# Performance work log

Hardware: AMD Instinct MI355X
Metric: run time of the kernel (lower is better)

Reference implementation:

```python
import jax, jax.numpy as jnp
import numpy as np

B, T, D = 4, 2048, 512
H, DK = 8, 64  # n_head, d_kv; inner_dim = H*DK = 512


def setup_inputs() -> dict:
    key = jax.random.key(0)
    ks = jax.random.split(key, 6)
    s = 1.0 / np.sqrt(D)
    return {
        "x": jax.random.normal(ks[0], (B, T, D), dtype=jnp.float32),
        "mask": jnp.zeros((B, 1, 1, T), dtype=jnp.float32),
        "position_bias": jax.random.normal(ks[1], (1, H, T, T), dtype=jnp.float32),
        "Wq": jax.random.normal(ks[2], (D, D), dtype=jnp.float32) * s,
        "Wk": jax.random.normal(ks[3], (D, D), dtype=jnp.float32) * s,
        "Wv": jax.random.normal(ks[4], (D, D), dtype=jnp.float32) * s,
        "Wo": jax.random.normal(ks[5], (D, D), dtype=jnp.float32) * s,
    }


def reference(x, mask, position_bias, Wq, Wk, Wv, Wo):
    # Linear projections (torch nn.Linear: y = x @ W.T), split into heads.
    q = (x @ Wq.T).reshape(B, T, H, DK).transpose(0, 2, 1, 3)  # [B,H,T,DK]
    k = (x @ Wk.T).reshape(B, T, H, DK).transpose(0, 2, 1, 3)  # [B,H,S,DK]
    v = (x @ Wv.T).reshape(B, T, H, DK).transpose(0, 2, 1, 3)  # [B,H,S,DK]
    # T5: no 1/sqrt(d_k) scaling; additive position bias + mask before softmax.
    scores = jnp.einsum("bhtd,bhsd->bhts", q, k) + position_bias + mask
    attn = jax.nn.softmax(scores.astype(jnp.float32), axis=-1).astype(q.dtype)
    # dropout is identity at inference
    y = jnp.einsum("bhts,bhsd->bhtd", attn, v)  # [B,H,T,DK]
    y = y.transpose(0, 2, 1, 3).reshape(B, T, H * DK)
    return y @ Wo.T
```

## Files before the change

kernel.cpp:

```cpp
#include <hip/hip_runtime.h>
#include <stdint.h>

typedef unsigned short u16;
typedef __attribute__((ext_vector_type(8))) _Float16 half8;
typedef __attribute__((ext_vector_type(4))) float f32x4;

#define L2E 1.4426950408889634f

#define NTOK 8192
#define DIM  512
#define TT   2048

__device__ __forceinline__ u16 f2h(float f) {
  _Float16 h = (_Float16)f;
  return __builtin_bit_cast(u16, h);
}

__device__ __forceinline__ void async16(const void* g, void* l) {
  __builtin_amdgcn_global_load_lds(
      (const __attribute__((address_space(1))) unsigned int*)g,
      (__attribute__((address_space(3))) unsigned int*)l, 16, 0, 0);
}

__global__ __launch_bounds__(256) void k_convert(
    const float* __restrict__ x, const float* __restrict__ wq,
    const float* __restrict__ wk, const float* __restrict__ wv,
    const float* __restrict__ wo, u16* __restrict__ xb) {
  size_t i = ((size_t)blockIdx.x * 256 + threadIdx.x) * 8;
  const float* src;
  u16* dst;
  size_t off;
  if (i < 4194304) {
    src = x; dst = xb; off = i;
  } else {
    size_t j = i - 4194304;
    int w = (int)(j >> 18);
    off = j & 262143;
    src = (w == 0) ? wq : (w == 1) ? wk : (w == 2) ? wv : wo;
    dst = xb + 4194304 + (size_t)w * 262144;
  }
  float4 a = *(const float4*)(src + off);
  float4 b = *(const float4*)(src + off + 4);
  uint4 pk;
  pk.x = (unsigned)f2h(a.x) | ((unsigned)f2h(a.y) << 16);
  pk.y = (unsigned)f2h(a.z) | ((unsigned)f2h(a.w) << 16);
  pk.z = (unsigned)f2h(b.x) | ((unsigned)f2h(b.y) << 16);
  pk.w = (unsigned)f2h(b.z) | ((unsigned)f2h(b.w) << 16);
  *(uint4*)(dst + off) = pk;
}

template <bool VSWAP>
__global__ __launch_bounds__(256) void k_proj(
    const u16* __restrict__ A, const u16* __restrict__ Wb,
    u16* __restrict__ Db) {
  const int tid = threadIdx.x;
  const int wave = tid >> 6, lane = tid & 63;
  const int quad = lane >> 4, l16 = lane & 15;
  const int wr = wave >> 1, wc = wave & 1;
  const int m0 = blockIdx.x * 128, n0 = blockIdx.y * 128;

  const u16* W;
  u16* D;
  if (VSWAP) {
    W = Wb + 2 * 262144;
    D = Db + 2 * (size_t)4194304;
  } else {
    int z = blockIdx.z;
    W = Wb + (size_t)z * 262144;
    D = Db + (size_t)z * 4194304;
  }

  __shared__ __align__(16) u16 As[128 * 64];
  __shared__ __align__(16) u16 Bs[128 * 64];

  f32x4 acc[4][4];
  for (int rt = 0; rt < 4; ++rt)
    for (int ct = 0; ct < 4; ++ct) acc[rt][ct] = (f32x4){0.f, 0.f, 0.f, 0.f};

  for (int kb = 0; kb < 8; ++kb) {
    const int k0 = kb * 64;
    for (int r = 0; r < 4; ++r) {
      int cid = r * 256 + tid;
      int row = cid >> 3, cl = cid & 7, cg = cl ^ (row & 7);
      async16(A + (size_t)(m0 + row) * DIM + k0 + cg * 8,
              &As[(r * 256 + wave * 64) * 8]);
    }
    for (int r = 0; r < 4; ++r) {
      int cid = r * 256 + tid;
      int row = cid >> 3, cl = cid & 7, cg = cl ^ (row & 7);
      async16(W + (size_t)(n0 + row) * DIM + k0 + cg * 8,
              &Bs[(r * 256 + wave * 64) * 8]);
    }
    __syncthreads();
    for (int kc = 0; kc < 2; ++kc) {
      half8 af[4], wf[4];
      for (int rt = 0; rt < 4; ++rt) {
        int row = wr * 64 + rt * 16 + l16;
        int c = (kc * 4 + quad) ^ (row & 7);
        af[rt] = *(const half8*)&As[row * 64 + c * 8];
      }
      for (int ct = 0; ct < 4; ++ct) {
        int row = wc * 64 + ct * 16 + l16;
        int c = (kc * 4 + quad) ^ (row & 7);
        wf[ct] = *(const half8*)&Bs[row * 64 + c * 8];
      }
      for (int rt = 0; rt < 4; ++rt)
        for (int ct = 0; ct < 4; ++ct)
          acc[rt][ct] = VSWAP
              ? __builtin_amdgcn_mfma_f32_16x16x32_f16(wf[ct], af[rt],
                                                       acc[rt][ct], 0, 0, 0)
              : __builtin_amdgcn_mfma_f32_16x16x32_f16(af[rt], wf[ct],
                                                       acc[rt][ct], 0, 0, 0);
    }
    __syncthreads();
  }

  for (int rt = 0; rt < 4; ++rt)
    for (int ct = 0; ct < 4; ++ct)
      for (int reg = 0; reg < 4; ++reg) {
        float v = acc[rt][ct][reg];
        if (!VSWAP) {
          int gm = m0 + wr * 64 + rt * 16 + quad * 4 + reg;
          int gn = n0 + wc * 64 + ct * 16 + l16;
          int bb = gm >> 11, t = gm & 2047, hh = gn >> 6, dk = gn & 63;
          D[(((size_t)(bb * 8 + hh) * TT + t) << 6) + dk] = f2h(v);
        } else {
          int feat = n0 + wc * 64 + ct * 16 + quad * 4 + reg;
          int tok  = m0 + wr * 64 + rt * 16 + l16;
          int bb = tok >> 11, t = tok & 2047, hh = feat >> 6, dk = feat & 63;
          D[(((size_t)(bb * 8 + hh) << 6) + dk) * TT + t] = f2h(v);
        }
      }
}

__global__ __launch_bounds__(256) void k_ogemm(
    const u16* __restrict__ A, const u16* __restrict__ W,
    float* __restrict__ Df) {
  const int tid = threadIdx.x;
  const int wave = tid >> 6, lane = tid & 63;
  const int quad = lane >> 4, l16 = lane & 15;
  const int wr = wave >> 1, wc = wave & 1;
  const int m0 = blockIdx.x * 64, n0 = blockIdx.y * 128;

  __shared__ __align__(16) u16 As[64 * 64];
  __shared__ __align__(16) u16 Bs[128 * 64];

  f32x4 acc[2][4];
  for (int rt = 0; rt < 2; ++rt)
    for (int ct = 0; ct < 4; ++ct) acc[rt][ct] = (f32x4){0.f, 0.f, 0.f, 0.f};

  for (int kb = 0; kb < 8; ++kb) {
    const int k0 = kb * 64;
    for (int r = 0; r < 2; ++r) {
      int cid = r * 256 + tid;
      int row = cid >> 3, cl = cid & 7, cg = cl ^ (row & 7);
      async16(A + (size_t)(m0 + row) * DIM + k0 + cg * 8,
              &As[(r * 256 + wave * 64) * 8]);
    }
    for (int r = 0; r < 4; ++r) {
      int cid = r * 256 + tid;
      int row = cid >> 3, cl = cid & 7, cg = cl ^ (row & 7);
      async16(W + (size_t)(n0 + row) * DIM + k0 + cg * 8,
              &Bs[(r * 256 + wave * 64) * 8]);
    }
    __syncthreads();
    for (int kc = 0; kc < 2; ++kc) {
      half8 af[2], wf[4];
      for (int rt = 0; rt < 2; ++rt) {
        int row = wr * 32 + rt * 16 + l16;
        int c = (kc * 4 + quad) ^ (row & 7);
        af[rt] = *(const half8*)&As[row * 64 + c * 8];
      }
      for (int ct = 0; ct < 4; ++ct) {
        int row = wc * 64 + ct * 16 + l16;
        int c = (kc * 4 + quad) ^ (row & 7);
        wf[ct] = *(const half8*)&Bs[row * 64 + c * 8];
      }
      for (int rt = 0; rt < 2; ++rt)
        for (int ct = 0; ct < 4; ++ct)
          acc[rt][ct] = __builtin_amdgcn_mfma_f32_16x16x32_f16(
              af[rt], wf[ct], acc[rt][ct], 0, 0, 0);
    }
    __syncthreads();
  }

  for (int rt = 0; rt < 2; ++rt)
    for (int ct = 0; ct < 4; ++ct)
      for (int reg = 0; reg < 4; ++reg) {
        int gm = m0 + wr * 32 + rt * 16 + quad * 4 + reg;
        int gn = n0 + wc * 64 + ct * 16 + l16;
        Df[(size_t)gm * DIM + gn] = acc[rt][ct][reg];
      }
}

__global__ __launch_bounds__(256, 4) void k_attn(
    const u16* __restrict__ Q, const u16* __restrict__ K,
    const u16* __restrict__ Vt, const float* __restrict__ bias,
    const float* __restrict__ mask, u16* __restrict__ Y) {
  const int tid = threadIdx.x;
  const int wv = tid >> 6;
  const int lane = tid & 63;
  const int quad = lane >> 4;
  const int l16 = lane & 15;

  const int bx = blockIdx.x;
  const int bh = bx >> 5;
  const int qt = bx & 31;
  const int b = bh >> 3, h = bh & 7;
  const int q0 = qt * 64;

  __shared__ __align__(16) u16 Ks[64 * 64];
  __shared__ __align__(16) u16 Vs[64 * 64];
  __shared__ __align__(16) u16 Pl[64 * 72];

  const int qrow = q0 + wv * 16 + l16;
  half8 qf[2];
  {
    size_t qoff = ((size_t)bh * TT + qrow) * 64;
    qf[0] = *(const half8*)(Q + qoff + quad * 8);
    qf[1] = *(const half8*)(Q + qoff + 32 + quad * 8);
  }

  const float* brow = bias + (size_t)h * TT * TT + (size_t)qrow * TT + quad * 4;
  const float* mrow = mask + (size_t)b * TT + quad * 4;

  float m_i = -1e30f, l_i = 0.f;
  f32x4 oacc[4];
  for (int ct = 0; ct < 4; ++ct) oacc[ct] = (f32x4){0.f, 0.f, 0.f, 0.f};

  f32x4 bL[4];
  for (int ct = 0; ct < 4; ++ct) bL[ct] = *(const f32x4*)(brow + ct * 16);

  for (int st = 0; st < 32; ++st) {
    const int s0 = st * 64;
    for (int r = 0; r < 2; ++r) {
      int cid = r * 256 + tid;
      int row = cid >> 3, cl = cid & 7, cg = cl ^ (row & 7);
      async16(K + ((size_t)bh * TT + s0 + row) * 64 + cg * 8,
              &Ks[(r * 256 + wv * 64) * 8]);
      async16(Vt + ((size_t)(bh * 64 + row)) * TT + s0 + cg * 8,
              &Vs[(r * 256 + wv * 64) * 8]);
    }
    f32x4 mL[4];
    for (int ct = 0; ct < 4; ++ct)
      mL[ct] = *(const f32x4*)(mrow + s0 + ct * 16);
    __syncthreads();

    f32x4 sacc[4];
    for (int ct = 0; ct < 4; ++ct) sacc[ct] = (f32x4){0.f, 0.f, 0.f, 0.f};
    __builtin_amdgcn_s_setprio(1);
    for (int kc = 0; kc < 2; ++kc) {
      half8 kf[4];
      for (int ct = 0; ct < 4; ++ct) {
        int row = ct * 16 + l16;
        int c = (kc * 4 + quad) ^ (row & 7);
        kf[ct] = *(const half8*)&Ks[row * 64 + c * 8];
      }
      for (int ct = 0; ct < 4; ++ct)
        sacc[ct] = __builtin_amdgcn_mfma_f32_16x16x32_f16(kf[ct], qf[kc],
                                                          sacc[ct], 0, 0, 0);
    }
    __builtin_amdgcn_s_setprio(0);

    float sv[4][4];
    for (int ct = 0; ct < 4; ++ct)
      for (int reg = 0; reg < 4; ++reg)
        sv[ct][reg] = sacc[ct][reg] + bL[ct][reg] + mL[ct][reg];

    {
      int sn = (st < 31) ? s0 + 64 : 0;
      for (int ct = 0; ct < 4; ++ct)
        bL[ct] = *(const f32x4*)(brow + sn + ct * 16);
    }

    float mc[4];
    for (int ct = 0; ct < 4; ++ct)
      mc[ct] = fmaxf(fmaxf(sv[ct][0], sv[ct][1]), fmaxf(sv[ct][2], sv[ct][3]));
    float mx = fmaxf(fmaxf(mc[0], mc[1]), fmaxf(mc[2], mc[3]));
    mx = fmaxf(mx, __shfl_xor(mx, 16));
    mx = fmaxf(mx, __shfl_xor(mx, 32));
    float mnew = fmaxf(m_i, mx);
    float alpha = __builtin_amdgcn_exp2f((m_i - mnew) * L2E);
    float nl2e = mnew * L2E;
    float rs = 0.f;
    for (int ct = 0; ct < 4; ++ct)
      for (int reg = 0; reg < 4; ++reg) {
        float p = __builtin_amdgcn_exp2f(sv[ct][reg] * L2E - nl2e);
        sv[ct][reg] = p;
        rs += p;
      }
    rs += __shfl_xor(rs, 16);
    rs += __shfl_xor(rs, 32);
    l_i = l_i * alpha + rs;
    m_i = mnew;
    for (int ct = 0; ct < 4; ++ct) {
      oacc[ct][0] *= alpha; oacc[ct][1] *= alpha;
      oacc[ct][2] *= alpha; oacc[ct][3] *= alpha;
    }

    for (int ct = 0; ct < 4; ++ct) {
      uint2 pk;
      pk.x = (unsigned)f2h(sv[ct][0]) | ((unsigned)f2h(sv[ct][1]) << 16);
      pk.y = (unsigned)f2h(sv[ct][2]) | ((unsigned)f2h(sv[ct][3]) << 16);
      *(uint2*)&Pl[(wv * 16 + l16) * 72 + ct * 16 + quad * 4] = pk;
    }
    asm volatile("s_waitcnt lgkmcnt(0)" ::: "memory");
    __builtin_amdgcn_sched_barrier(0);

    __builtin_amdgcn_s_setprio(1);
    for (int kc = 0; kc < 2; ++kc) {
      half8 pf = *(const half8*)&Pl[(wv * 16 + l16) * 72 + kc * 32 + quad * 8];
      half8 vf[4];
      for (int ct = 0; ct < 4; ++ct) {
        int row = ct * 16 + l16;
        int c = (kc * 4 + quad) ^ (row & 7);
        vf[ct] = *(const half8*)&Vs[row * 64 + c * 8];
      }
      for (int ct = 0; ct < 4; ++ct)
        oacc[ct] = __builtin_amdgcn_mfma_f32_16x16x32_f16(vf[ct], pf,
                                                          oacc[ct], 0, 0, 0);
    }
    __builtin_amdgcn_s_setprio(0);
    __syncthreads();
  }

  float inv = 1.f / l_i;
  size_t ybase = ((size_t)(b * TT + qrow)) * DIM + h * 64 + quad * 4;
  for (int ct = 0; ct < 4; ++ct) {
    uint2 pk;
    pk.x = (unsigned)f2h(oacc[ct][0] * inv) |
           ((unsigned)f2h(oacc[ct][1] * inv) << 16);
    pk.y = (unsigned)f2h(oacc[ct][2] * inv) |
           ((unsigned)f2h(oacc[ct][3] * inv) << 16);
    *(uint2*)(Y + ybase + ct * 16) = pk;
  }
}

extern "C" void kernel_launch(void* const* d_in, const int* in_sizes, int n_in,
                              void* d_out, int out_size, void* d_ws, size_t ws_size,
                              hipStream_t stream) {
  const float* x    = (const float*)d_in[0];
  const float* mask = (const float*)d_in[1];
  const float* bias = (const float*)d_in[2];
  const float* Wq   = (const float*)d_in[3];
  const float* Wk   = (const float*)d_in[4];
  const float* Wv   = (const float*)d_in[5];
  const float* Wo   = (const float*)d_in[6];
  (void)Wk; (void)Wv;

  u16* xb  = (u16*)d_ws;
  u16* wb  = xb + 4194304;
  u16* qkv = wb + 4 * 262144;
  u16* yb  = qkv + 3 * (size_t)4194304;

  k_convert<<<2560, 256, 0, stream>>>(x, Wq, Wk, Wv, Wo, xb);
  k_proj<false><<<dim3(64, 4, 2), 256, 0, stream>>>(xb, wb, qkv);
  k_proj<true><<<dim3(64, 4), 256, 0, stream>>>(xb, wb, qkv);
  k_attn<<<1024, 256, 0, stream>>>(qkv, qkv + 4194304,
                                   qkv + 2 * (size_t)4194304, bias, mask, yb);
  k_ogemm<<<dim3(128, 4), 256, 0, stream>>>(yb, wb + 3 * 262144, (float*)d_out);
}
```

Before: 322.1 us.

## Double-buffer K/V tiles, lazy softmax rescale, swizzle P, reorder blocks by head

The attention kernel now double-buffers the K and V shared-memory tiles, issuing async loads for the next tile before computing on the current one. This removes the load-then-barrier stall at the top of each iteration. Several other changes ride along: the online-softmax rescale of the output and running sum is skipped unless the row max grows by more than 8, and the P scratch buffer uses an XOR swizzle in place of padding. Block indices are also remapped so that consecutive blocks cover different heads of the same batch. The cost is double the K/V shared memory, which may lower occupancy. The lazy rescale lets exponentials exceed 1 (up to about e^8), which stays within fp16 range.

Result: slower. 342.4 us (+6.3%).

```diff
diff --git a/kernel.cpp b/kernel.cpp
--- a/kernel.cpp
+++ b/kernel.cpp
@@ -204,14 +204,16 @@
   const int l16 = lane & 15;
 
   const int bx = blockIdx.x;
-  const int bh = bx >> 5;
-  const int qt = bx & 31;
-  const int b = bh >> 3, h = bh & 7;
+  const int h = bx & 7;
+  const int lid = bx >> 3;
+  const int b = lid >> 5;
+  const int qt = lid & 31;
+  const int bh = b * 8 + h;
   const int q0 = qt * 64;
 
-  __shared__ __align__(16) u16 Ks[64 * 64];
-  __shared__ __align__(16) u16 Vs[64 * 64];
-  __shared__ __align__(16) u16 Pl[64 * 72];
+  __shared__ __align__(16) u16 Ks[2][64 * 64];
+  __shared__ __align__(16) u16 Vs[2][64 * 64];
+  __shared__ __align__(16) u16 Pl[64 * 64];
 
   const int qrow = q0 + wv * 16 + l16;
   half8 qf[2];
@@ -228,101 +230,118 @@
   f32x4 oacc[4];
   for (int ct = 0; ct < 4; ++ct) oacc[ct] = (f32x4){0.f, 0.f, 0.f, 0.f};
 
-  f32x4 bL[4];
-  for (int ct = 0; ct < 4; ++ct) bL[ct] = *(const f32x4*)(brow + ct * 16);
-
-  for (int st = 0; st < 32; ++st) {
-    const int s0 = st * 64;
-    for (int r = 0; r < 2; ++r) {
-      int cid = r * 256 + tid;
-      int row = cid >> 3, cl = cid & 7, cg = cl ^ (row & 7);
-      async16(K + ((size_t)bh * TT + s0 + row) * 64 + cg * 8,
-              &Ks[(r * 256 + wv * 64) * 8]);
-      async16(Vt + ((size_t)(bh * 64 + row)) * TT + s0 + cg * 8,
-              &Vs[(r * 256 + wv * 64) * 8]);
-    }
-    f32x4 mL[4];
-    for (int ct = 0; ct < 4; ++ct)
-      mL[ct] = *(const f32x4*)(mrow + s0 + ct * 16);
-    __syncthreads();
-
-    f32x4 sacc[4];
-    for (int ct = 0; ct < 4; ++ct) sacc[ct] = (f32x4){0.f, 0.f, 0.f, 0.f};
-    __builtin_amdgcn_s_setprio(1);
-    for (int kc = 0; kc < 2; ++kc) {
-      half8 kf[4];
-      for (int ct = 0; ct < 4; ++ct) {
-        int row = ct * 16 + l16;
-        int c = (kc * 4 + quad) ^ (row & 7);
-        kf[ct] = *(const half8*)&Ks[row * 64 + c * 8];
-      }
-      for (int ct = 0; ct < 4; ++ct)
-        sacc[ct] = __builtin_amdgcn_mfma_f32_16x16x32_f16(kf[ct], qf[kc],
-                                                          sacc[ct], 0, 0, 0);
-    }
-    __builtin_amdgcn_s_setprio(0);
-
-    float sv[4][4];
-    for (int ct = 0; ct < 4; ++ct)
-      for (int reg = 0; reg < 4; ++reg)
-        sv[ct][reg] = sacc[ct][reg] + bL[ct][reg] + mL[ct][reg];
-
-    {
-      int sn = (st < 31) ? s0 + 64 : 0;
-      for (int ct = 0; ct < 4; ++ct)
-        bL[ct] = *(const f32x4*)(brow + sn + ct * 16);
-    }
-
-    float mc[4];
-    for (int ct = 0; ct < 4; ++ct)
-      mc[ct] = fmaxf(fmaxf(sv[ct][0], sv[ct][1]), fmaxf(sv[ct][2], sv[ct][3]));
-    float mx = fmaxf(fmaxf(mc[0], mc[1]), fmaxf(mc[2], mc[3]));
-    mx = fmaxf(mx, __shfl_xor(mx, 16));
-    mx = fmaxf(mx, __shfl_xor(mx, 32));
-    float mnew = fmaxf(m_i, mx);
-    float alpha = __builtin_amdgcn_exp2f((m_i - mnew) * L2E);
-    float nl2e = mnew * L2E;
-    float rs = 0.f;
-    for (int ct = 0; ct < 4; ++ct)
-      for (int reg = 0; reg < 4; ++reg) {
-        float p = __builtin_amdgcn_exp2f(sv[ct][reg] * L2E - nl2e);
-        sv[ct][reg] = p;
-        rs += p;
-      }
-    rs += __shfl_xor(rs, 16);
-    rs += __shfl_xor(rs, 32);
-    l_i = l_i * alpha + rs;
-    m_i = mnew;
-    for (int ct = 0; ct < 4; ++ct) {
-      oacc[ct][0] *= alpha; oacc[ct][1] *= alpha;
-      oacc[ct][2] *= alpha; oacc[ct][3] *= alpha;
-    }
-
-    for (int ct = 0; ct < 4; ++ct) {
-      uint2 pk;
-      pk.x = (unsigned)f2h(sv[ct][0]) | ((unsigned)f2h(sv[ct][1]) << 16);
-      pk.y = (unsigned)f2h(sv[ct][2]) | ((unsigned)f2h(sv[ct][3]) << 16);
-      *(uint2*)&Pl[(wv * 16 + l16) * 72 + ct * 16 + quad * 4] = pk;
-    }
-    asm volatile("s_waitcnt lgkmcnt(0)" ::: "memory");
-    __builtin_amdgcn_sched_barrier(0);
-
-    __builtin_amdgcn_s_setprio(1);
-    for (int kc = 0; kc < 2; ++kc) {
-      half8 pf = *(const half8*)&Pl[(wv * 16 + l16) * 72 + kc * 32 + quad * 8];
-      half8 vf[4];
-      for (int ct = 0; ct < 4; ++ct) {
-        int row = ct * 16 + l16;
-        int c = (kc * 4 + quad) ^ (row & 7);
-        vf[ct] = *(const half8*)&Vs[row * 64 + c * 8];
-      }
-      for (int ct = 0; ct < 4; ++ct)
-        oacc[ct] = __builtin_amdgcn_mfma_f32_16x16x32_f16(vf[ct], pf,
-                                                          oacc[ct], 0, 0, 0);
-    }
-    __builtin_amdgcn_s_setprio(0);
-    __syncthreads();
-  }
+  const int prow = wv * 16 + l16;
+  const int r7x = (l16 & 7) << 4;
+  char* plb = (char*)Pl + prow * 128;
+
+#define STAGE(BUF, S0)                                                  \
+  for (int r = 0; r < 2; ++r) {                                         \
+    int cid = r * 256 + tid;                                            \
+    int row = cid >> 3, cl = cid & 7, cg = cl ^ (row & 7);              \
+    async16(K + ((size_t)bh * TT + (S0) + row) * 64 + cg * 8,           \
+            &Ks[BUF][(r * 256 + wv * 64) * 8]);                         \
+    async16(Vt + ((size_t)(bh * 64 + row)) * TT + (S0) + cg * 8,        \
+            &Vs[BUF][(r * 256 + wv * 64) * 8]);                         \
+  }
+
+  f32x4 bA[4], bB[4];
+  STAGE(0, 0);
+  for (int ct = 0; ct < 4; ++ct) bA[ct] = *(const f32x4*)(brow + ct * 16);
+  __syncthreads();
+
+#define TILE(ST, CUR, BU, BF)                                               \
+  {                                                                         \
+    const int s0 = (ST) * 64;                                               \
+    if ((ST) < 31) {                                                        \
+      STAGE((CUR) ^ 1, s0 + 64);                                            \
+      for (int ct = 0; ct < 4; ++ct)                                        \
+        BF[ct] = *(const f32x4*)(brow + s0 + 64 + ct * 16);                 \
+    }                                                                       \
+    f32x4 mL[4];                                                            \
+    for (int ct = 0; ct < 4; ++ct)                                          \
+      mL[ct] = *(const f32x4*)(mrow + s0 + ct * 16);                        \
+                                \
+    f32x4 sacc[4];                                                          \
+    for (int ct = 0; ct < 4; ++ct) sacc[ct] = (f32x4){0.f, 0.f, 0.f, 0.f};  \
+    __builtin_amdgcn_s_setprio(1);                                          \
+    for (int kc = 0; kc < 2; ++kc) {                                        \
+      half8 kf[4];                                                          \
+      for (int ct = 0; ct < 4; ++ct) {                                      \
+        int row = ct * 16 + l16;                                            \
+        int c = (kc * 4 + quad) ^ (row & 7);                                \
+        kf[ct] = *(const half8*)&Ks[CUR][row * 64 + c * 8];                 \
+      }                                                                     \
+      for (int ct = 0; ct < 4; ++ct)                                        \
+        sacc[ct] = __builtin_amdgcn_mfma_f32_16x16x32_f16(kf[ct], qf[kc],   \
+                                                          sacc[ct], 0, 0, 0); \
+    }                                                                       \
+    __builtin_amdgcn_s_setprio(0);                                          \
+    float sv[4][4];                                                         \
+    for (int ct = 0; ct < 4; ++ct)                                          \
+      for (int rg = 0; rg < 4; ++rg)                                        \
+        sv[ct][rg] = sacc[ct][rg] + BU[ct][rg] + mL[ct][rg];                \
+                     \
+    float mc0 = fmaxf(fmaxf(sv[0][0], sv[0][1]), fmaxf(sv[0][2], sv[0][3])); \
+    float mc1 = fmaxf(fmaxf(sv[1][0], sv[1][1]), fmaxf(sv[1][2], sv[1][3])); \
+    float mc2 = fmaxf(fmaxf(sv[2][0], sv[2][1]), fmaxf(sv[2][2], sv[2][3])); \
+    float mc3 = fmaxf(fmaxf(sv[3][0], sv[3][1]), fmaxf(sv[3][2], sv[3][3])); \
+    float mx = fmaxf(fmaxf(mc0, mc1), fmaxf(mc2, mc3));                     \
+    mx = fmaxf(mx, __shfl_xor(mx, 16));                                     \
+    mx = fmaxf(mx, __shfl_xor(mx, 32));                                     \
+    if (!__all(mx <= m_i + 8.f)) {                                          \
+      float mnew = fmaxf(m_i, mx);                                          \
+      float alpha = __builtin_amdgcn_exp2f((m_i - mnew) * L2E);             \
+      l_i *= alpha;                                                         \
+      m_i = mnew;                                                           \
+      for (int ct = 0; ct < 4; ++ct) {                                      \
+        oacc[ct][0] *= alpha; oacc[ct][1] *= alpha;                         \
+        oacc[ct][2] *= alpha; oacc[ct][3] *= alpha;                         \
+      }                                                                     \
+    }                                                                       \
+    float nl2e = m_i * L2E;                                                 \
+    float rs = 0.f;                                                         \
+    for (int ct = 0; ct < 4; ++ct)                                          \
+      for (int rg = 0; rg < 4; ++rg) {                                      \
+        float p = __builtin_amdgcn_exp2f(sv[ct][rg] * L2E - nl2e);          \
+        sv[ct][rg] = p;                                                     \
+        rs += p;                                                            \
+      }                                                                     \
+    rs += __shfl_xor(rs, 16);                                               \
+    rs += __shfl_xor(rs, 32);                                               \
+    l_i += rs;                                                              \
+                            \
+    for (int ct = 0; ct < 4; ++ct) {                                        \
+      uint2 pk;                                                             \
+      pk.x = (unsigned)f2h(sv[ct][0]) | ((unsigned)f2h(sv[ct][1]) << 16);   \
+      pk.y = (unsigned)f2h(sv[ct][2]) | ((unsigned)f2h(sv[ct][3]) << 16);   \
+      *(uint2*)(plb + ((ct * 32 + quad * 8) ^ r7x)) = pk;                   \
+    }                                                                       \
+    asm volatile("s_waitcnt lgkmcnt(0)" ::: "memory");                      \
+    __builtin_amdgcn_sched_barrier(0);                                      \
+                            \
+    __builtin_amdgcn_s_setprio(1);                                          \
+    for (int kc = 0; kc < 2; ++kc) {                                        \
+      half8 pf = *(const half8*)(plb + ((kc * 64 + quad * 16) ^ r7x));      \
+      half8 vf[4];                                                          \
+      for (int ct = 0; ct < 4; ++ct) {                                      \
+        int row = ct * 16 + l16;                                            \
+        int c = (kc * 4 + quad) ^ (row & 7);                                \
+        vf[ct] = *(const half8*)&Vs[CUR][row * 64 + c * 8];                 \
+      }                                                                     \
+      for (int ct = 0; ct < 4; ++ct)                                        \
+        oacc[ct] = __builtin_amdgcn_mfma_f32_16x16x32_f16(vf[ct], pf,       \
+                                                          oacc[ct], 0, 0, 0); \
+    }                                                                       \
+    __builtin_amdgcn_s_setprio(0);                                          \
+    __syncthreads();                                                        \
+  }
+
+  for (int st2 = 0; st2 < 16; ++st2) {
+    TILE(2 * st2, 0, bA, bB);
+    TILE(2 * st2 + 1, 1, bB, bA);
+  }
+#undef TILE
+#undef STAGE
 
   float inv = 1.f / l_i;
   size_t ybase = ((size_t)(b * TT + qrow)) * DIM + h * 64 + quad * 4;
```

## Process 128-key blocks per barrier in attention, reorder grid by head, vectorize QKV stores

Applied to the files above, without the earlier changes.

The attention kernel now stages 128 keys of K and V per iteration and processes them in two 64-key halves, which halves the number of block-wide barriers and async load rounds. Block indexing is remapped so consecutive blocks cover different heads, and the P scratch buffer now uses an XOR swizzle instead of padding. In the projection kernel the non-swapped path stores four packed halves per write instead of scalar stores. These changes cost more LDS per block, which may lower occupancy, and bias/mask prefetch is no longer overlapped with the previous iteration's compute.

Result: slower. 347.5 us (+7.9%).

```diff
diff --git a/kernel.cpp b/kernel.cpp
--- a/kernel.cpp
+++ b/kernel.cpp
@@ -106,31 +106,34 @@
       }
       for (int rt = 0; rt < 4; ++rt)
         for (int ct = 0; ct < 4; ++ct)
-          acc[rt][ct] = VSWAP
-              ? __builtin_amdgcn_mfma_f32_16x16x32_f16(wf[ct], af[rt],
-                                                       acc[rt][ct], 0, 0, 0)
-              : __builtin_amdgcn_mfma_f32_16x16x32_f16(af[rt], wf[ct],
-                                                       acc[rt][ct], 0, 0, 0);
+          acc[rt][ct] = __builtin_amdgcn_mfma_f32_16x16x32_f16(
+              wf[ct], af[rt], acc[rt][ct], 0, 0, 0);
     }
     __syncthreads();
   }
 
   for (int rt = 0; rt < 4; ++rt)
-    for (int ct = 0; ct < 4; ++ct)
-      for (int reg = 0; reg < 4; ++reg) {
-        float v = acc[rt][ct][reg];
-        if (!VSWAP) {
-          int gm = m0 + wr * 64 + rt * 16 + quad * 4 + reg;
-          int gn = n0 + wc * 64 + ct * 16 + l16;
-          int bb = gm >> 11, t = gm & 2047, hh = gn >> 6, dk = gn & 63;
-          D[(((size_t)(bb * 8 + hh) * TT + t) << 6) + dk] = f2h(v);
-        } else {
+    for (int ct = 0; ct < 4; ++ct) {
+      if (!VSWAP) {
+        int feat0 = n0 + wc * 64 + ct * 16 + quad * 4;
+        int tok   = m0 + wr * 64 + rt * 16 + l16;
+        int bb = tok >> 11, t = tok & 2047, hh = feat0 >> 6, dk0 = feat0 & 63;
+        uint2 pk;
+        pk.x = (unsigned)f2h(acc[rt][ct][0]) |
+               ((unsigned)f2h(acc[rt][ct][1]) << 16);
+        pk.y = (unsigned)f2h(acc[rt][ct][2]) |
+               ((unsigned)f2h(acc[rt][ct][3]) << 16);
+        *(uint2*)&D[(((size_t)(bb * 8 + hh) * TT + t) << 6) + dk0] = pk;
+      } else {
+        for (int reg = 0; reg < 4; ++reg) {
           int feat = n0 + wc * 64 + ct * 16 + quad * 4 + reg;
           int tok  = m0 + wr * 64 + rt * 16 + l16;
           int bb = tok >> 11, t = tok & 2047, hh = feat >> 6, dk = feat & 63;
-          D[(((size_t)(bb * 8 + hh) << 6) + dk) * TT + t] = f2h(v);
+          D[(((size_t)(bb * 8 + hh) << 6) + dk) * TT + t] =
+              f2h(acc[rt][ct][reg]);
         }
       }
+    }
 }
 
 __global__ __launch_bounds__(256) void k_ogemm(
@@ -204,14 +207,16 @@
   const int l16 = lane & 15;
 
   const int bx = blockIdx.x;
-  const int bh = bx >> 5;
-  const int qt = bx & 31;
-  const int b = bh >> 3, h = bh & 7;
+  const int h = bx & 7;
+  const int lid = bx >> 3;
+  const int b = lid >> 5;
+  const int qt = lid & 31;
+  const int bh = b * 8 + h;
   const int q0 = qt * 64;
 
-  __shared__ __align__(16) u16 Ks[64 * 64];
-  __shared__ __align__(16) u16 Vs[64 * 64];
-  __shared__ __align__(16) u16 Pl[64 * 72];
+  __shared__ __align__(16) u16 Ks[128 * 64];
+  __shared__ __align__(16) u16 Vs[64 * 128];
+  __shared__ __align__(16) u16 Pl[64 * 64];
 
   const int qrow = q0 + wv * 16 + l16;
   half8 qf[2];
@@ -228,99 +233,108 @@
   f32x4 oacc[4];
   for (int ct = 0; ct < 4; ++ct) oacc[ct] = (f32x4){0.f, 0.f, 0.f, 0.f};
 
-  f32x4 bL[4];
-  for (int ct = 0; ct < 4; ++ct) bL[ct] = *(const f32x4*)(brow + ct * 16);
-
-  for (int st = 0; st < 32; ++st) {
-    const int s0 = st * 64;
-    for (int r = 0; r < 2; ++r) {
+  const int prow = wv * 16 + l16;
+  const int r7x = (l16 & 7) << 4;
+  char* plb = (char*)Pl + prow * 128;
+
+  for (int sb = 0; sb < 16; ++sb) {
+    const int s0 = sb * 128;
+    for (int r = 0; r < 4; ++r) {
       int cid = r * 256 + tid;
       int row = cid >> 3, cl = cid & 7, cg = cl ^ (row & 7);
       async16(K + ((size_t)bh * TT + s0 + row) * 64 + cg * 8,
               &Ks[(r * 256 + wv * 64) * 8]);
+    }
+    for (int r = 0; r < 4; ++r) {
+      int cid = r * 256 + tid;
+      int row = cid >> 4, cl = cid & 15, cg = cl ^ (row & 7);
       async16(Vt + ((size_t)(bh * 64 + row)) * TT + s0 + cg * 8,
               &Vs[(r * 256 + wv * 64) * 8]);
     }
-    f32x4 mL[4];
-    for (int ct = 0; ct < 4; ++ct)
+    f32x4 bL[8], mL[8];
+    for (int ct = 0; ct < 8; ++ct) {
+      bL[ct] = *(const f32x4*)(brow + s0 + ct * 16);
       mL[ct] = *(const f32x4*)(mrow + s0 + ct * 16);
-    __syncthreads();
-
-    f32x4 sacc[4];
-    for (int ct = 0; ct < 4; ++ct) sacc[ct] = (f32x4){0.f, 0.f, 0.f, 0.f};
-    __builtin_amdgcn_s_setprio(1);
-    for (int kc = 0; kc < 2; ++kc) {
-      half8 kf[4];
+    }
+    __syncthreads();
+    for (int ct = 0; ct < 8; ++ct) {
+      bL[ct][0] += mL[ct][0]; bL[ct][1] += mL[ct][1];
+      bL[ct][2] += mL[ct][2]; bL[ct][3] += mL[ct][3];
+    }
+
+#pragma unroll
+    for (int hf = 0; hf < 2; ++hf) {
+      f32x4 sacc[4];
+      for (int ct = 0; ct < 4; ++ct) sacc[ct] = (f32x4){0.f, 0.f, 0.f, 0.f};
+      __builtin_amdgcn_s_setprio(1);
+      for (int kc = 0; kc < 2; ++kc) {
+        half8 kf[4];
+        for (int ct = 0; ct < 4; ++ct) {
+          int row = hf * 64 + ct * 16 + l16;
+          int c = (kc * 4 + quad) ^ (row & 7);
+          kf[ct] = *(const half8*)&Ks[row * 64 + c * 8];
+        }
+        for (int ct = 0; ct < 4; ++ct)
+          sacc[ct] = __builtin_amdgcn_mfma_f32_16x16x32_f16(kf[ct], qf[kc],
+                                                            sacc[ct], 0, 0, 0);
+      }
+      __builtin_amdgcn_s_setprio(0);
+
+      float sv[4][4];
+      for (int ct = 0; ct < 4; ++ct)
+        for (int rg = 0; rg < 4; ++rg)
+          sv[ct][rg] = sacc[ct][rg] + bL[hf * 4 + ct][rg];
+
+      float mc0 = fmaxf(fmaxf(sv[0][0], sv[0][1]), fmaxf(sv[0][2], sv[0][3]));
+      float mc1 = fmaxf(fmaxf(sv[1][0], sv[1][1]), fmaxf(sv[1][2], sv[1][3]));
+      float mc2 = fmaxf(fmaxf(sv[2][0], sv[2][1]), fmaxf(sv[2][2], sv[2][3]));
+      float mc3 = fmaxf(fmaxf(sv[3][0], sv[3][1]), fmaxf(sv[3][2], sv[3][3]));
+      float mx = fmaxf(fmaxf(mc0, mc1), fmaxf(mc2, mc3));
+      mx = fmaxf(mx, __shfl_xor(mx, 16));
+      mx = fmaxf(mx, __shfl_xor(mx, 32));
+      float mnew = fmaxf(m_i, mx);
+      float alpha = __builtin_amdgcn_exp2f((m_i - mnew) * L2E);
+      float nl2e = mnew * L2E;
+      float rs = 0.f;
+      for (int ct = 0; ct < 4; ++ct)
+        for (int rg = 0; rg < 4; ++rg) {
+          float p = __builtin_amdgcn_exp2f(sv[ct][rg] * L2E - nl2e);
+          sv[ct][rg] = p;
+          rs += p;
+        }
+      rs += __shfl_xor(rs, 16);
+      rs += __shfl_xor(rs, 32);
+      l_i = l_i * alpha + rs;
+      m_i = mnew;
       for (int ct = 0; ct < 4; ++ct) {
-        int row = ct * 16 + l16;
-        int c = (kc * 4 + quad) ^ (row & 7);
-        kf[ct] = *(const half8*)&Ks[row * 64 + c * 8];
-      }
-      for (int ct = 0; ct < 4; ++ct)
-        sacc[ct] = __builtin_amdgcn_mfma_f32_16x16x32_f16(kf[ct], qf[kc],
-                                                          sacc[ct], 0, 0, 0);
-    }
-    __builtin_amdgcn_s_setprio(0);
-
-    float sv[4][4];
-    for (int ct = 0; ct < 4; ++ct)
-      for (int reg = 0; reg < 4; ++reg)
-        sv[ct][reg] = sacc[ct][reg] + bL[ct][reg] + mL[ct][reg];
-
-    {
-      int sn = (st < 31) ? s0 + 64 : 0;
-      for (int ct = 0; ct < 4; ++ct)
-        bL[ct] = *(const f32x4*)(brow + sn + ct * 16);
-    }
-
-    float mc[4];
-    for (int ct = 0; ct < 4; ++ct)
-      mc[ct] = fmaxf(fmaxf(sv[ct][0], sv[ct][1]), fmaxf(sv[ct][2], sv[ct][3]));
-    float mx = fmaxf(fmaxf(mc[0], mc[1]), fmaxf(mc[2], mc[3]));
-    mx = fmaxf(mx, __shfl_xor(mx, 16));
-    mx = fmaxf(mx, __shfl_xor(mx, 32));
-    float mnew = fmaxf(m_i, mx);
-    float alpha = __builtin_amdgcn_exp2f((m_i - mnew) * L2E);
-    float nl2e = mnew * L2E;
-    float rs = 0.f;
-    for (int ct = 0; ct < 4; ++ct)
-      for (int reg = 0; reg < 4; ++reg) {
-        float p = __builtin_amdgcn_exp2f(sv[ct][reg] * L2E - nl2e);
-        sv[ct][reg] = p;
-        rs += p;
-      }
-    rs += __shfl_xor(rs, 16);
-    rs += __shfl_xor(rs, 32);
-    l_i = l_i * alpha + rs;
-    m_i = mnew;
-    for (int ct = 0; ct < 4; ++ct) {
-      oacc[ct][0] *= alpha; oacc[ct][1] *= alpha;
-      oacc[ct][2] *= alpha; oacc[ct][3] *= alpha;
-    }
-
-    for (int ct = 0; ct < 4; ++ct) {
-      uint2 pk;
-      pk.x = (unsigned)f2h(sv[ct][0]) | ((unsigned)f2h(sv[ct][1]) << 16);
-      pk.y = (unsigned)f2h(sv[ct][2]) | ((unsigned)f2h(sv[ct][3]) << 16);
-      *(uint2*)&Pl[(wv * 16 + l16) * 72 + ct * 16 + quad * 4] = pk;
-    }
-    asm volatile("s_waitcnt lgkmcnt(0)" ::: "memory");
-    __builtin_amdgcn_sched_barrier(0);
-
-    __builtin_amdgcn_s_setprio(1);
-    for (int kc = 0; kc < 2; ++kc) {
-      half8 pf = *(const half8*)&Pl[(wv * 16 + l16) * 72 + kc * 32 + quad * 8];
-      half8 vf[4];
+        oacc[ct][0] *= alpha; oacc[ct][1] *= alpha;
+        oacc[ct][2] *= alpha; oacc[ct][3] *= alpha;
+      }
+
       for (int ct = 0; ct < 4; ++ct) {
-        int row = ct * 16 + l16;
-        int c = (kc * 4 + quad) ^ (row & 7);
-        vf[ct] = *(const half8*)&Vs[row * 64 + c * 8];
-      }
-      for (int ct = 0; ct < 4; ++ct)
-        oacc[ct] = __builtin_amdgcn_mfma_f32_16x16x32_f16(vf[ct], pf,
-                                                          oacc[ct], 0, 0, 0);
-    }
-    __builtin_amdgcn_s_setprio(0);
+        uint2 pk;
+        pk.x = (unsigned)f2h(sv[ct][0]) | ((unsigned)f2h(sv[ct][1]) << 16);
+        pk.y = (unsigned)f2h(sv[ct][2]) | ((unsigned)f2h(sv[ct][3]) << 16);
+        *(uint2*)(plb + ((ct * 32 + quad * 8) ^ r7x)) = pk;
+      }
+      asm volatile("s_waitcnt lgkmcnt(0)" ::: "memory");
+      __builtin_amdgcn_sched_barrier(0);
+
+      __builtin_amdgcn_s_setprio(1);
+      for (int kc = 0; kc < 2; ++kc) {
+        half8 pf = *(const half8*)(plb + ((kc * 64 + quad * 16) ^ r7x));
+        half8 vf[4];
+        for (int ct = 0; ct < 4; ++ct) {
+          int row = ct * 16 + l16;
+          int chunk = hf * 8 + ((kc * 4 + quad) ^ (row & 7));
+          vf[ct] = *(const half8*)&Vs[row * 128 + chunk * 8];
+        }
+        for (int ct = 0; ct < 4; ++ct)
+          oacc[ct] = __builtin_amdgcn_mfma_f32_16x16x32_f16(vf[ct], pf,
+                                                            oacc[ct], 0, 0, 0);
+      }
+      __builtin_amdgcn_s_setprio(0);
+    }
     __syncthreads();
   }
 
```

## Merge QKV projections into one launch, vectorize epilogue stores, enlarge output GEMM tile

Applied to the files above, without the earlier changes.

Merges the two projection launches into a single grid of 64x12 blocks, where the block's column index selects Q, K or V. All three now use the swapped MFMA operand order, so each lane holds four consecutive features. That lets Q/K results go out as packed 8-byte stores and the output GEMM write float4 rows. The output GEMM tile grows from 64x128 to 128x128, halving its block count (256 blocks), which raises per-block reuse but may underfill the GPU. The attention kernel only has a variable renamed.

Result: no change. 325.3 us (+1.0%).

```diff
diff --git a/kernel.cpp b/kernel.cpp
--- a/kernel.cpp
+++ b/kernel.cpp
@@ -49,26 +49,20 @@
   *(uint4*)(dst + off) = pk;
 }
 
-template <bool VSWAP>
-__global__ __launch_bounds__(256) void k_proj(
+__global__ __launch_bounds__(256) void k_projall(
     const u16* __restrict__ A, const u16* __restrict__ Wb,
     u16* __restrict__ Db) {
   const int tid = threadIdx.x;
   const int wave = tid >> 6, lane = tid & 63;
   const int quad = lane >> 4, l16 = lane & 15;
   const int wr = wave >> 1, wc = wave & 1;
-  const int m0 = blockIdx.x * 128, n0 = blockIdx.y * 128;
-
-  const u16* W;
-  u16* D;
-  if (VSWAP) {
-    W = Wb + 2 * 262144;
-    D = Db + 2 * (size_t)4194304;
-  } else {
-    int z = blockIdx.z;
-    W = Wb + (size_t)z * 262144;
-    D = Db + (size_t)z * 4194304;
-  }
+  const int m0 = blockIdx.x * 128;
+  const int gn0 = blockIdx.y * 128;
+  const int z = gn0 >> 9;
+  const int n0 = gn0 & 511;
+
+  const u16* W = Wb + (size_t)z * 262144;
+  u16* D = Db + (size_t)z * 4194304;
 
   __shared__ __align__(16) u16 As[128 * 64];
   __shared__ __align__(16) u16 Bs[128 * 64];
@@ -106,31 +100,31 @@
       }
       for (int rt = 0; rt < 4; ++rt)
         for (int ct = 0; ct < 4; ++ct)
-          acc[rt][ct] = VSWAP
-              ? __builtin_amdgcn_mfma_f32_16x16x32_f16(wf[ct], af[rt],
-                                                       acc[rt][ct], 0, 0, 0)
-              : __builtin_amdgcn_mfma_f32_16x16x32_f16(af[rt], wf[ct],
-                                                       acc[rt][ct], 0, 0, 0);
+          acc[rt][ct] = __builtin_amdgcn_mfma_f32_16x16x32_f16(
+              wf[ct], af[rt], acc[rt][ct], 0, 0, 0);
     }
     __syncthreads();
   }
 
   for (int rt = 0; rt < 4; ++rt)
-    for (int ct = 0; ct < 4; ++ct)
-      for (int reg = 0; reg < 4; ++reg) {
-        float v = acc[rt][ct][reg];
-        if (!VSWAP) {
-          int gm = m0 + wr * 64 + rt * 16 + quad * 4 + reg;
-          int gn = n0 + wc * 64 + ct * 16 + l16;
-          int bb = gm >> 11, t = gm & 2047, hh = gn >> 6, dk = gn & 63;
-          D[(((size_t)(bb * 8 + hh) * TT + t) << 6) + dk] = f2h(v);
-        } else {
-          int feat = n0 + wc * 64 + ct * 16 + quad * 4 + reg;
-          int tok  = m0 + wr * 64 + rt * 16 + l16;
-          int bb = tok >> 11, t = tok & 2047, hh = feat >> 6, dk = feat & 63;
-          D[(((size_t)(bb * 8 + hh) << 6) + dk) * TT + t] = f2h(v);
+    for (int ct = 0; ct < 4; ++ct) {
+      int feat0 = n0 + wc * 64 + ct * 16 + quad * 4;
+      int tok   = m0 + wr * 64 + rt * 16 + l16;
+      int bb = tok >> 11, t = tok & 2047, hh = feat0 >> 6, dk0 = feat0 & 63;
+      if (z < 2) {
+        uint2 pk;
+        pk.x = (unsigned)f2h(acc[rt][ct][0]) |
+               ((unsigned)f2h(acc[rt][ct][1]) << 16);
+        pk.y = (unsigned)f2h(acc[rt][ct][2]) |
+               ((unsigned)f2h(acc[rt][ct][3]) << 16);
+        *(uint2*)&D[(((size_t)(bb * 8 + hh) * TT + t) << 6) + dk0] = pk;
+      } else {
+        for (int reg = 0; reg < 4; ++reg) {
+          D[(((size_t)(bb * 8 + hh) << 6) + dk0 + reg) * TT + t] =
+              f2h(acc[rt][ct][reg]);
         }
       }
+    }
 }
 
 __global__ __launch_bounds__(256) void k_ogemm(
@@ -140,18 +134,18 @@
   const int wave = tid >> 6, lane = tid & 63;
   const int quad = lane >> 4, l16 = lane & 15;
   const int wr = wave >> 1, wc = wave & 1;
-  const int m0 = blockIdx.x * 64, n0 = blockIdx.y * 128;
-
-  __shared__ __align__(16) u16 As[64 * 64];
+  const int m0 = blockIdx.x * 128, n0 = blockIdx.y * 128;
+
+  __shared__ __align__(16) u16 As[128 * 64];
   __shared__ __align__(16) u16 Bs[128 * 64];
 
-  f32x4 acc[2][4];
-  for (int rt = 0; rt < 2; ++rt)
+  f32x4 acc[4][4];
+  for (int rt = 0; rt < 4; ++rt)
     for (int ct = 0; ct < 4; ++ct) acc[rt][ct] = (f32x4){0.f, 0.f, 0.f, 0.f};
 
   for (int kb = 0; kb < 8; ++kb) {
     const int k0 = kb * 64;
-    for (int r = 0; r < 2; ++r) {
+    for (int r = 0; r < 4; ++r) {
       int cid = r * 256 + tid;
       int row = cid >> 3, cl = cid & 7, cg = cl ^ (row & 7);
       async16(A + (size_t)(m0 + row) * DIM + k0 + cg * 8,
@@ -165,9 +159,9 @@
     }
     __syncthreads();
     for (int kc = 0; kc < 2; ++kc) {
-      half8 af[2], wf[4];
-      for (int rt = 0; rt < 2; ++rt) {
-        int row = wr * 32 + rt * 16 + l16;
+      half8 af[4], wf[4];
+      for (int rt = 0; rt < 4; ++rt) {
+        int row = wr * 64 + rt * 16 + l16;
         int c = (kc * 4 + quad) ^ (row & 7);
         af[rt] = *(const half8*)&As[row * 64 + c * 8];
       }
@@ -176,21 +170,22 @@
         int c = (kc * 4 + quad) ^ (row & 7);
         wf[ct] = *(const half8*)&Bs[row * 64 + c * 8];
       }
-      for (int rt = 0; rt < 2; ++rt)
+      for (int rt = 0; rt < 4; ++rt)
         for (int ct = 0; ct < 4; ++ct)
           acc[rt][ct] = __builtin_amdgcn_mfma_f32_16x16x32_f16(
-              af[rt], wf[ct], acc[rt][ct], 0, 0, 0);
-    }
-    __syncthreads();
-  }
-
-  for (int rt = 0; rt < 2; ++rt)
-    for (int ct = 0; ct < 4; ++ct)
-      for (int reg = 0; reg < 4; ++reg) {
-        int gm = m0 + wr * 32 + rt * 16 + quad * 4 + reg;
-        int gn = n0 + wc * 64 + ct * 16 + l16;
-        Df[(size_t)gm * DIM + gn] = acc[rt][ct][reg];
-      }
+              wf[ct], af[rt], acc[rt][ct], 0, 0, 0);
+    }
+    __syncthreads();
+  }
+
+  for (int rt = 0; rt < 4; ++rt)
+    for (int ct = 0; ct < 4; ++ct) {
+      int feat0 = n0 + wc * 64 + ct * 16 + quad * 4;
+      int tok   = m0 + wr * 64 + rt * 16 + l16;
+      *(float4*)&Df[(size_t)tok * DIM + feat0] =
+          (float4){acc[rt][ct][0], acc[rt][ct][1],
+                   acc[rt][ct][2], acc[rt][ct][3]};
+    }
 }
 
 __global__ __launch_bounds__(256, 4) void k_attn(
@@ -264,8 +259,8 @@
 
     float sv[4][4];
     for (int ct = 0; ct < 4; ++ct)
-      for (int reg = 0; reg < 4; ++reg)
-        sv[ct][reg] = sacc[ct][reg] + bL[ct][reg] + mL[ct][reg];
+      for (int rg = 0; rg < 4; ++rg)
+        sv[ct][rg] = sacc[ct][rg] + bL[ct][rg] + mL[ct][rg];
 
     {
       int sn = (st < 31) ? s0 + 64 : 0;
@@ -284,9 +279,9 @@
     float nl2e = mnew * L2E;
     float rs = 0.f;
     for (int ct = 0; ct < 4; ++ct)
-      for (int reg = 0; reg < 4; ++reg) {
-        float p = __builtin_amdgcn_exp2f(sv[ct][reg] * L2E - nl2e);
-        sv[ct][reg] = p;
+      for (int rg = 0; rg < 4; ++rg) {
+        float p = __builtin_amdgcn_exp2f(sv[ct][rg] * L2E - nl2e);
+        sv[ct][rg] = p;
         rs += p;
       }
     rs += __shfl_xor(rs, 16);
@@ -354,9 +349,8 @@
   u16* yb  = qkv + 3 * (size_t)4194304;
 
   k_convert<<<2560, 256, 0, stream>>>(x, Wq, Wk, Wv, Wo, xb);
-  k_proj<false><<<dim3(64, 4, 2), 256, 0, stream>>>(xb, wb, qkv);
-  k_proj<true><<<dim3(64, 4), 256, 0, stream>>>(xb, wb, qkv);
+  k_projall<<<dim3(64, 12), 256, 0, stream>>>(xb, wb, qkv);
   k_attn<<<1024, 256, 0, stream>>>(qkv, qkv + 4194304,
                                    qkv + 2 * (size_t)4194304, bias, mask, yb);
-  k_ogemm<<<dim3(128, 4), 256, 0, stream>>>(yb, wb + 3 * 262144, (float*)d_out);
-}
+  k_ogemm<<<dim3(64, 4), 256, 0, stream>>>(yb, wb + 3 * 262144, (float*)d_out);
+}
```
